# Optimization experiments

Measured on AMD Instinct MI355X. Metric: run time of the kernel, lower is better.

Reference implementation:

```python
import jax, jax.numpy as jnp
import numpy as np

B, N, E, D, H, C, U = 512, 256, 1024, 256, 256, 8, 64
MARGIN_T, RISK_T, SCALE = 0.2, 0.6, 0.1
NEG = -1.0e9


def setup_inputs() -> dict:
    key = jax.random.key(0)
    ks = jax.random.split(key, 30)
    s = 0.02
    inp = dict(
        features=jax.random.normal(ks[0], (B, D), jnp.float32),
        centered_scores=jax.random.normal(ks[1], (B, N), jnp.float32),
        margin=jax.random.uniform(ks[2], (B,), jnp.float32),
        boundary_risk=jax.random.uniform(ks[3], (B,), jnp.float32),
        edge_sensitivity=jax.random.normal(ks[4], (B, E), jnp.float32),
        coords=jax.random.normal(ks[5], (B, N, C), jnp.float32),
        uncertainty=jax.random.uniform(ks[6], (B, U), jnp.float32),
        Wc1=jax.random.normal(ks[7], (D, H), jnp.float32) * s,
        bc1=jnp.zeros((H,), jnp.float32),
        Wc2=jax.random.normal(ks[8], (H, H), jnp.float32) * s,
        bc2=jnp.zeros((H,), jnp.float32),
        Wn1=jax.random.normal(ks[9], (H + C + 2, H), jnp.float32) * s,
        bn1=jnp.zeros((H,), jnp.float32),
        Wn2=jax.random.normal(ks[10], (H, 1), jnp.float32) * s,
        bn2=jnp.zeros((1,), jnp.float32),
        We1=jax.random.normal(ks[11], (H + C + 2, H), jnp.float32) * s,
        be1=jnp.zeros((H,), jnp.float32),
        We2=jax.random.normal(ks[12], (H, 1), jnp.float32) * s,
        be2=jnp.zeros((1,), jnp.float32),
        Wg=jax.random.normal(ks[13], (H, 1), jnp.float32) * s,
        bg=jnp.zeros((1,), jnp.float32),
        action_mask=jax.random.bernoulli(ks[14], 0.8, (B, N)),
        edge_mask=jax.random.bernoulli(ks[15], 0.8, (B, E)),
        actions=jax.random.randint(ks[16], (B, N), 0, U, jnp.int32),
        edges=jax.random.randint(ks[17], (B, E, 2), 0, N, jnp.int32),
    )
    return inp


def _mlp2(x, W1, b1, W2, b2):
    return jax.nn.relu(x @ W1 + b1) @ W2 + b2


def reference(features, centered_scores, margin, boundary_risk, edge_sensitivity,
              coords, uncertainty, Wc1, bc1, Wc2, bc2, Wn1, bn1, Wn2, bn2,
              We1, be1, We2, be2, Wg, bg, action_mask, edge_mask, actions, edges):
    amf = action_mask.astype(jnp.float32)
    emf = edge_mask.astype(jnp.float32)

    # context MLP
    h = jax.nn.relu(jax.nn.relu(features @ Wc1 + bc1) @ Wc2 + bc2)  # [B,H]

    low_margin = (margin < MARGIN_T).astype(jnp.float32)
    high_risk = (boundary_risk > RISK_T).astype(jnp.float32)
    learned_gate = jax.nn.sigmoid((h @ Wg + bg)[:, 0])
    refine_gate = jnp.maximum(jnp.maximum(low_margin, high_risk),
                              (learned_gate > 0.5).astype(jnp.float32))  # [B]

    # node features: [B,N,H+C+2]
    act = jnp.clip(actions, 0, U - 1)
    unc_g = jnp.take_along_axis(uncertainty, act, axis=1)  # [B,N]
    h_n = jnp.broadcast_to(h[:, None, :], (B, N, H))
    node_feats = jnp.concatenate(
        [h_n, coords, centered_scores[..., None], unc_g[..., None]], axis=-1)
    node_delta = _mlp2(node_feats, Wn1, bn1, Wn2, bn2)[..., 0] * amf  # [B,N]

    # edge features: gather src/dst coords
    e = jnp.clip(edges, 0, N - 1)
    src_c = jnp.take_along_axis(coords, e[:, :, 0:1], axis=1)  # [B,E,C]
    dst_c = jnp.take_along_axis(coords, e[:, :, 1:2], axis=1)  # [B,E,C]
    h_e = jnp.broadcast_to(h[:, None, :], (B, E, H))
    edge_feats = jnp.concatenate(
        [h_e, dst_c - src_c, edge_sensitivity[..., None], emf[..., None]], axis=-1)
    edge_delta = _mlp2(edge_feats, We1, be1, We2, be2)[..., 0] * emf  # [B,E]

    gate_node = refine_gate[:, None]
    refined_scores = (centered_scores + gate_node * SCALE * node_delta) * amf
    denom = jnp.clip(amf.sum(-1, keepdims=True), 1.0, None)  # [B,1]
    refined_scores = (refined_scores - refined_scores.sum(-1, keepdims=True) / denom) * amf

    refined_edge = (edge_sensitivity + gate_node * SCALE * edge_delta) * emf

    masked_top = jnp.where(action_mask, refined_scores, NEG)
    top_vals, top_idx = jax.lax.top_k(masked_top, 2)
    refined_margin = top_vals[:, 0] - top_vals[:, 1]

    # masked per-batch variance of refined_edge (biased), 0 if <=1 valid entry
    cnt = emf.sum(-1)
    cnt_c = jnp.clip(cnt, 1.0, None)
    mean = (refined_edge * emf).sum(-1) / cnt_c
    var = (emf * (refined_edge - mean[:, None]) ** 2).sum(-1) / cnt_c
    edge_var = jnp.where(cnt > 1.0, var, 0.0)

    unc_term = (unc_g * amf).sum(-1) / denom[:, 0]
    refined_risk = jnp.clip(
        jax.nn.sigmoid(-refined_margin) + 0.2 * edge_var + 0.1 * unc_term, 0.0, 1.0)

    return (refined_scores, refined_margin, refined_edge,
            top_idx[:, 0], refined_risk, refine_gate)
```

## Files before the change

kernel.cpp:

```cpp
#include <hip/hip_runtime.h>
#include <math.h>

#define B 512
#define N 256
#define E 1024
#define D 256
#define H 256
#define C 8
#define U 64

typedef __fp16 h2 __attribute__((ext_vector_type(2)));
union UF { float f; h2 h; unsigned u; };

__device__ __forceinline__ float bc_f(h2 h) { UF u; u.h = h; return u.f; }
__device__ __forceinline__ h2 bc_h(float f) { UF u; u.f = f; return u.h; }

#if __has_builtin(__builtin_amdgcn_cvt_pkrtz)
__device__ __forceinline__ h2 pkh(float a, float b) { return __builtin_amdgcn_cvt_pkrtz(a, b); }
#else
__device__ __forceinline__ h2 pkh(float a, float b) { h2 r; r.x = (__fp16)a; r.y = (__fp16)b; return r; }
#endif

#if __has_builtin(__builtin_amdgcn_fdot2)
__device__ __forceinline__ float FDOT2(h2 a, h2 b, float c) { return __builtin_amdgcn_fdot2(a, b, c, false); }
#else
__device__ __forceinline__ float FDOT2(h2 a, h2 b, float c) {
    return fmaf((float)a.x, (float)b.x, fmaf((float)a.y, (float)b.y, c));
}
#endif

__device__ __forceinline__ float mask_val(const void* m, long i, int flag) {
    if (flag == 1) return ((const unsigned char*)m)[i] ? 1.f : 0.f;
    if (flag == 2) return (((const float*)m)[i] != 0.f) ? 1.f : 0.f;
    return ((const int*)m)[i] ? 1.f : 0.f;
}

__global__ __launch_bounds__(512) void k_h(
    const float* __restrict__ feat,
    const float* __restrict__ Wc1, const float* __restrict__ bc1,
    const float* __restrict__ Wc2, const float* __restrict__ bc2,
    const float* __restrict__ Wn1, const float* __restrict__ bn1,
    const float* __restrict__ We1, const float* __restrict__ be1,
    const float* __restrict__ Wg,  const float* __restrict__ bg,
    const float* __restrict__ margin, const float* __restrict__ brisk,
    const unsigned int* __restrict__ amask_words,
    float* __restrict__ base_n, float* __restrict__ base_e,
    float* __restrict__ out_gate, int* __restrict__ flag,
    float* __restrict__ node_delta, float* __restrict__ out2)
{
    __shared__ __align__(16) float sF[2][256];
    __shared__ __align__(16) float sH[2][256];
    __shared__ float red[512];
    __shared__ int cls0, cls1;

    int t = threadIdx.x;
    int w = t >> 8;
    int c = t & 255;
    int b0 = blockIdx.x * 2;
    int b = b0 + w;

    {
        int idx = blockIdx.x * 512 + t;
        node_delta[idx] = 0.f;
        ((float4*)out2)[idx] = make_float4(0.f, 0.f, 0.f, 0.f);
    }

    if (blockIdx.x == 0) {
        if (t == 0) { cls0 = 0; cls1 = 0; }
        __syncthreads();
        if (t < 256) {
            unsigned int wd = amask_words[t];
            if (wd != 0u && wd != 1u) {
                if (wd == 0x3f800000u) atomicOr(&cls1, 1);
                else                   atomicOr(&cls0, 1);
            }
        }
        __syncthreads();
        if (t == 0) *flag = cls0 ? 1 : (cls1 ? 2 : 0);
    }

    sF[w][c] = feat[(long)b * D + c];
    __syncthreads();

    {
        float acc[4] = {bc1[c], 0.f, 0.f, 0.f};
        const float* Wp = Wc1 + c;
        for (int d0 = 0; d0 < D; d0 += 16) {
            float wv[16];
            #pragma unroll
            for (int k = 0; k < 16; k++) wv[k] = Wp[(long)(d0 + k) * H];
            #pragma unroll
            for (int k = 0; k < 16; k++)
                acc[k & 3] = fmaf(sF[w][d0 + k], wv[k], acc[k & 3]);
        }
        sH[w][c] = fmaxf((acc[0] + acc[1]) + (acc[2] + acc[3]), 0.f);
    }
    __syncthreads();

    {
        float acc[4] = {bc2[c], 0.f, 0.f, 0.f};
        const float* Wp = Wc2 + c;
        for (int d0 = 0; d0 < H; d0 += 16) {
            float wv[16];
            #pragma unroll
            for (int k = 0; k < 16; k++) wv[k] = Wp[(long)(d0 + k) * H];
            #pragma unroll
            for (int k = 0; k < 16; k++)
                acc[k & 3] = fmaf(sH[w][d0 + k], wv[k], acc[k & 3]);
        }
        float a = fmaxf((acc[0] + acc[1]) + (acc[2] + acc[3]), 0.f);
        __syncthreads();
        sF[w][c] = a;
    }
    __syncthreads();

    red[t] = sF[w][c] * Wg[c];
    __syncthreads();
    for (int s = 128; s > 0; s >>= 1) {
        if (c < s) red[t] += red[t + s];
        __syncthreads();
    }
    if (c == 0) {
        float lg = 1.f / (1.f + expf(-(red[t] + bg[0])));
        out_gate[b] = ((margin[b] < 0.2f) || (brisk[b] > 0.6f) || (lg > 0.5f)) ? 1.f : 0.f;
    }

    {
        const float* W3  = w ? (We1 + c) : (Wn1 + c);
        float bias       = w ? be1[c]    : bn1[c];
        float* dst       = w ? base_e    : base_n;
        float aA[2] = {bias, 0.f};
        float aB[2] = {bias, 0.f};
        for (int d0 = 0; d0 < H; d0 += 16) {
            float wv[16];
            #pragma unroll
            for (int k = 0; k < 16; k++) wv[k] = W3[(long)(d0 + k) * H];
            #pragma unroll
            for (int k = 0; k < 16; k++) {
                aA[k & 1] = fmaf(sF[0][d0 + k], wv[k], aA[k & 1]);
                aB[k & 1] = fmaf(sF[1][d0 + k], wv[k], aB[k & 1]);
            }
        }
        dst[(long)b0 * H + c]       = aA[0] + aA[1];
        dst[(long)(b0 + 1) * H + c] = aB[0] + aB[1];
    }
}

__global__ __launch_bounds__(256, 2) void k_ne(
    const float* __restrict__ cs, const float* __restrict__ coords,
    const float* __restrict__ unc, const int* __restrict__ actions,
    const float* __restrict__ Wn1, const float* __restrict__ Wn2,
    const float* __restrict__ base_n,
    const float* __restrict__ es, const int* __restrict__ edges,
    const float* __restrict__ We1, const float* __restrict__ We2,
    const float* __restrict__ base_e,
    const float* __restrict__ gate,
    float* __restrict__ node_delta, float* __restrict__ out2)
{
    __shared__ __align__(16) float smem[3840];
    int t = threadIdx.x;
    int w = t >> 6, lane = t & 63;

    if (blockIdx.x < 512) {
        int rg = blockIdx.x >> 2;
        int jq = blockIdx.x & 3;
        int b0 = rg * 4;
        float* pack = smem;
        float* sB   = smem + 768;

        {
            int i = t;
            #pragma unroll
            for (int s = 0; s < 3; s++, i += 256) {
                int j = i / 12, k = i - j * 12;
                int jj = jq * 64 + j;
                float v;
                if (k < 10)       v = Wn1[(long)(H + k) * H + jj];
                else if (k == 10) v = Wn2[jj];
                else              v = 0.f;
                pack[i] = v;
            }
            int r = t >> 6, j = t & 63;
            sB[r * 64 + j] = base_n[(long)(b0 + r) * H + jq * 64 + j];
        }
        __syncthreads();

        int b = b0 + w;
        float g = gate[b];
        if (g != 0.f) {
            float f8v[4], ug[4], acc[4];
            float f0[4], f1[4], f2[4], f3[4], f4[4], f5[4], f6[4], f7[4];
            #pragma unroll
            for (int q = 0; q < 4; q++) {
                int n = q * 64 + lane;
                const float4* cp = (const float4*)(coords + ((long)b * N + n) * C);
                float4 c0 = cp[0], c1 = cp[1];
                f0[q] = c0.x; f1[q] = c0.y; f2[q] = c0.z; f3[q] = c0.w;
                f4[q] = c1.x; f5[q] = c1.y; f6[q] = c1.z; f7[q] = c1.w;
                f8v[q] = cs[(long)b * N + n];
                int a = actions[(long)b * N + n];
                a = min(max(a, 0), U - 1);
                ug[q] = unc[(long)b * U + a];
                acc[q] = 0.f;
            }

            const float* sBw = sB + w * 64;
            #pragma unroll 4
            for (int j = 0; j < 64; j++) {
                const float* pj = pack + j * 12;
                float4 wa = *(const float4*)(pj);
                float4 wb = *(const float4*)(pj + 4);
                float4 wc = *(const float4*)(pj + 8);
                float bse = sBw[j];
                #pragma unroll
                for (int q = 0; q < 4; q++) {
                    float zA = fmaf(f0[q], wa.x, bse);
                    zA = fmaf(f1[q], wa.y, zA);
                    zA = fmaf(f2[q], wa.z, zA);
                    zA = fmaf(f3[q], wa.w, zA);
                    float zB = f4[q] * wb.x;
                    zB = fmaf(f5[q], wb.y, zB);
                    zB = fmaf(f6[q], wb.z, zB);
                    zB = fmaf(f7[q], wb.w, zB);
                    zB = fmaf(f8v[q], wc.x, zB);
                    zB = fmaf(ug[q], wc.y, zB);
                    acc[q] = fmaf(fmaxf(zA + zB, 0.f), wc.z, acc[q]);
                }
            }

            #pragma unroll
            for (int q = 0; q < 4; q++)
                atomicAdd(&node_delta[(long)b * N + q * 64 + lane], acc[q]);
        }
    } else {
        int eb = blockIdx.x - 512;
        int b = eb >> 2, jq = eb & 3;
        float g = gate[b];
        if (g == 0.f) return;

        float*  A4 = smem;
        float2* B2 = (float2*)(smem + 256);
        float*  sC = smem + 768;

        {
            const float4* g4 = (const float4*)(coords + (long)b * N * C);
            float4 c0 = g4[2 * t], c1 = g4[2 * t + 1];
            float4* d0 = (float4*)(sC + t * 12);
            d0[0] = c0; d0[1] = c1;
        }
        if (t < 64) {
            int j = jq * 64 + t;
            float w0 = We1[(long)(H + 0) * H + j];
            float w1 = We1[(long)(H + 1) * H + j];
            float w2 = We1[(long)(H + 2) * H + j];
            float w3 = We1[(long)(H + 3) * H + j];
            float w4 = We1[(long)(H + 4) * H + j];
            float w5 = We1[(long)(H + 5) * H + j];
            float w6 = We1[(long)(H + 6) * H + j];
            float w7 = We1[(long)(H + 7) * H + j];
            float w8 = We1[(long)(H + 8) * H + j];
            float w9 = We1[(long)(H + 9) * H + j];
            float we2 = We2[j];
            float bse = base_e[(long)b * H + j] + w9;
            float4 av;
            av.x = bc_f(pkh(w0, w1)); av.y = bc_f(pkh(w2, w3));
            av.z = bc_f(pkh(w4, w5)); av.w = bc_f(pkh(w6, w7));
            ((float4*)A4)[t] = av;
            B2[t] = make_float2(bc_f(pkh(w8, we2)), bse);
        }
        __syncthreads();

        float p01[4], p23[4], p45[4], p67[4], pes[4], acc[4];
        #pragma unroll
        for (int q = 0; q < 4; q++) {
            long idx = (long)b * E + w * 256 + q * 64 + lane;
            int2 ev = ((const int2*)edges)[idx];
            int s0 = min(max(ev.x, 0), N - 1);
            int d0 = min(max(ev.y, 0), N - 1);
            const float4* cs4 = (const float4*)(sC + s0 * 12);
            const float4* cd4 = (const float4*)(sC + d0 * 12);
            float4 sa = cs4[0], sb = cs4[1];
            float4 da = cd4[0], db = cd4[1];
            p01[q] = bc_f(pkh(da.x - sa.x, da.y - sa.y));
            p23[q] = bc_f(pkh(da.z - sa.z, da.w - sa.w));
            p45[q] = bc_f(pkh(db.x - sb.x, db.y - sb.y));
            p67[q] = bc_f(pkh(db.z - sb.z, db.w - sb.w));
            pes[q] = bc_f(pkh(es[idx], 0.f));
            acc[q] = 0.f;
        }

        const float4* A4v = (const float4*)A4;
        #pragma unroll 4
        for (int j = 0; j < 64; j++) {
            float4 av = A4v[j];
            float2 bv = B2[j];
            h2 w01 = bc_h(av.x), w23 = bc_h(av.y);
            h2 w45 = bc_h(av.z), w67 = bc_h(av.w);
            h2 w8x = bc_h(bv.x);
            float we2f = (float)(w8x.y);
            float bse = bv.y;
            #pragma unroll
            for (int q = 0; q < 4; q++) {
                float z = FDOT2(bc_h(p01[q]), w01, bse);
                z = FDOT2(bc_h(p23[q]), w23, z);
                z = FDOT2(bc_h(p45[q]), w45, z);
                z = FDOT2(bc_h(p67[q]), w8x, z);
                acc[q] = acc[q];
                z = FDOT2(bc_h(p67[q]), w67, FDOT2(bc_h(p45[q]), w45,
                    FDOT2(bc_h(p23[q]), w23, FDOT2(bc_h(p01[q]), w01, bse))));
                z = FDOT2(bc_h(pes[q]), w8x, z);
                acc[q] = fmaf(fmaxf(z, 0.f), we2f, acc[q]);
            }
        }

        #pragma unroll
        for (int q = 0; q < 4; q++)
            atomicAdd(&out2[(long)b * E + w * 256 + q * 64 + lane], acc[q]);
    }
}

__global__ __launch_bounds__(512) void k_fin2(
    const void* __restrict__ amask, const void* __restrict__ emask,
    const int* __restrict__ actions, const float* __restrict__ unc,
    const float* __restrict__ cs, const float* __restrict__ es,
    const float* __restrict__ bn2, const float* __restrict__ be2,
    const float* __restrict__ gate, const int* __restrict__ flagp,
    const float* __restrict__ node_delta,
    float* __restrict__ out0, float* __restrict__ out1,
    float* __restrict__ out2, float* __restrict__ out3,
    float* __restrict__ out4)
{
    __shared__ float sRisk;
    __shared__ float sS1[8], sCe[8], sVar[8];
    int t = threadIdx.x;
    int w = t >> 6, lane = t & 63;
    int b = blockIdx.x;
    int flag = *flagp;
    float g = gate[b];

    float re[4], emv[4];

    if (w == 0) {
        float b2v = bn2[0];
        float raw[4], amv[4], ug[4];
        #pragma unroll
        for (int q = 0; q < 4; q++) {
            long idx = (long)b * N + q * 64 + lane;
            amv[q] = mask_val(amask, idx, flag);
            float csv = cs[idx];
            int a = actions[idx];
            a = min(max(a, 0), U - 1);
            ug[q] = unc[(long)b * U + a];
            float nd = (node_delta[idx] + b2v) * amv[q];
            raw[q] = (csv + g * 0.1f * nd) * amv[q];
        }

        float s = 0.f, cn = 0.f, su = 0.f;
        #pragma unroll
        for (int q = 0; q < 4; q++) {
            s += raw[q]; cn += amv[q]; su += ug[q] * amv[q];
        }
        #pragma unroll
        for (int m = 1; m < 64; m <<= 1) {
            s  += __shfl_xor(s, m);
            cn += __shfl_xor(cn, m);
            su += __shfl_xor(su, m);
        }
        float denom = fmaxf(cn, 1.f);
        float mu = s / denom;

        float masked[4];
        #pragma unroll
        for (int q = 0; q < 4; q++) {
            float rs = (raw[q] - mu) * amv[q];
            out0[(long)b * N + q * 64 + lane] = rs;
            masked[q] = (amv[q] != 0.f) ? rs : -1e9f;
        }

        float v1 = masked[0]; int i1 = lane; float v2 = -1e9f;
        #pragma unroll
        for (int q = 1; q < 4; q++) {
            float mv = masked[q]; int mi = q * 64 + lane;
            if (mv > v1) { v2 = v1; v1 = mv; i1 = mi; }
            else v2 = fmaxf(v2, mv);
        }
        #pragma unroll
        for (int m = 1; m < 64; m <<= 1) {
            float ov1 = __shfl_xor(v1, m);
            int   oi1 = __shfl_xor(i1, m);
            float ov2 = __shfl_xor(v2, m);
            bool ow = (ov1 > v1) || (ov1 == v1 && oi1 < i1);
            float lv  = ow ? v1 : ov1;
            float wv2 = ow ? ov2 : v2;
            if (ow) { v1 = ov1; i1 = oi1; }
            v2 = fmaxf(lv, wv2);
        }

        if (lane == 0) {
            float rmargin = v1 - v2;
            out1[b] = rmargin;
            out3[b] = (float)i1;
            float sig = 1.f / (1.f + expf(rmargin));
            sRisk = sig + 0.1f * (su / denom);
            sS1[0] = 0.f; sCe[0] = 0.f;
        }
    } else if (w >= 4) {
        float be2v = be2[0];
        int eq = w - 4;
        float S1 = 0.f, ce = 0.f;
        #pragma unroll
        for (int q = 0; q < 4; q++) {
            long idx = (long)b * E + eq * 256 + q * 64 + lane;
            emv[q] = mask_val(emask, idx, flag);
            float delta = out2[idx] + be2v;
            float r = es[idx] + g * 0.1f * delta;
            re[q] = (emv[q] != 0.f) ? r : 0.f;
            out2[idx] = re[q];
            S1 += re[q]; ce += emv[q];
        }
        #pragma unroll
        for (int m = 1; m < 64; m <<= 1) {
            S1 += __shfl_xor(S1, m);
            ce += __shfl_xor(ce, m);
        }
        if (lane == 0) { sS1[w] = S1; sCe[w] = ce; }
    } else {
        if (lane == 0) { sS1[w] = 0.f; sCe[w] = 0.f; }
    }
    __syncthreads();

    float S1t = sS1[4] + sS1[5] + sS1[6] + sS1[7];
    float cet = sCe[4] + sCe[5] + sCe[6] + sCe[7];
    float mean = S1t / fmaxf(cet, 1.f);

    if (w >= 4) {
        float v = 0.f;
        #pragma unroll
        for (int q = 0; q < 4; q++) {
            float dd = re[q] - mean;
            v = fmaf(emv[q] * dd, dd, v);
        }
        #pragma unroll
        for (int m = 1; m < 64; m <<= 1) v += __shfl_xor(v, m);
        if (lane == 0) sVar[w] = v;
    } else {
        if (lane == 0) sVar[w] = 0.f;
    }
    __syncthreads();

    if (t == 0) {
        float vt = sVar[4] + sVar[5] + sVar[6] + sVar[7];
        float var = vt / fmaxf(cet, 1.f);
        float ev = (cet > 1.f) ? var : 0.f;
        float r = sRisk + 0.2f * ev;
        out4[b] = fminf(fmaxf(r, 0.f), 1.f);
    }
}

extern "C" void kernel_launch(void* const* d_in, const int* in_sizes, int n_in,
                              void* d_out, int out_size, void* d_ws, size_t ws_size,
                              hipStream_t stream) {
    const float* feat   = (const float*)d_in[0];
    const float* cs     = (const float*)d_in[1];
    const float* marg   = (const float*)d_in[2];
    const float* brisk  = (const float*)d_in[3];
    const float* es     = (const float*)d_in[4];
    const float* coords = (const float*)d_in[5];
    const float* unc    = (const float*)d_in[6];
    const float* Wc1    = (const float*)d_in[7];
    const float* bc1    = (const float*)d_in[8];
    const float* Wc2    = (const float*)d_in[9];
    const float* bc2    = (const float*)d_in[10];
    const float* Wn1    = (const float*)d_in[11];
    const float* bn1    = (const float*)d_in[12];
    const float* Wn2    = (const float*)d_in[13];
    const float* bn2    = (const float*)d_in[14];
    const float* We1    = (const float*)d_in[15];
    const float* be1    = (const float*)d_in[16];
    const float* We2    = (const float*)d_in[17];
    const float* be2    = (const float*)d_in[18];
    const float* Wg     = (const float*)d_in[19];
    const float* bg     = (const float*)d_in[20];
    const void*  amask  = d_in[21];
    const void*  emask  = d_in[22];
    const int*   actions= (const int*)d_in[23];
    const int*   edges  = (const int*)d_in[24];

    float* out0 = (float*)d_out;
    float* out1 = out0 + (long)B * N;
    float* out2 = out1 + B;
    float* out3 = out2 + (long)B * E;
    float* out4 = out3 + B;
    float* out5 = out4 + B;

    float* base_n     = (float*)d_ws;
    float* base_e     = base_n + (long)B * H;
    float* node_delta = base_e + (long)B * H;
    int*   flag       = (int*)(node_delta + (long)B * N);

    k_h<<<B / 2, 512, 0, stream>>>(feat, Wc1, bc1, Wc2, bc2, Wn1, bn1, We1, be1,
                                   Wg, bg, marg, brisk,
                                   (const unsigned int*)amask,
                                   base_n, base_e, out5, flag,
                                   node_delta, out2);
    k_ne<<<512 + 4 * B, 256, 0, stream>>>(cs, coords, unc, actions,
                                          Wn1, Wn2, base_n,
                                          es, edges,
                                          We1, We2, base_e,
                                          out5, node_delta, out2);
    k_fin2<<<B, 512, 0, stream>>>(amask, emask, actions, unc, cs, es,
                                  bn2, be2, out5, flag, node_delta,
                                  out0, out1, out2, out3, out4);
}
```

Before: 69.95 us.

## Split context MLP kernel into three wider-parallel kernels and drop redundant FDOT chain

The single context-MLP kernel, which ran 256 blocks of 512 threads and handled two rows per block through three dependent matmuls, is split into three kernels. Each new kernel handles 4 rows by 64 output columns per block, giving 512 to 1024 blocks. The gate logit is now reduced with wavefront shuffles into per-quarter partial sums and finished in the third kernel. Separately, the edge inner loop drops a duplicated FDOT2 chain that recomputed z. The split adds two extra launches plus workspace round-trips for intermediates, in exchange for more parallelism and less per-block serial work.

```diff
diff --git a/kernel.cpp b/kernel.cpp
--- a/kernel.cpp
+++ b/kernel.cpp
@@ -35,114 +35,149 @@
     return ((const int*)m)[i] ? 1.f : 0.f;
 }
 
-__global__ __launch_bounds__(512) void k_h(
+__global__ __launch_bounds__(256) void k_h1(
     const float* __restrict__ feat,
     const float* __restrict__ Wc1, const float* __restrict__ bc1,
-    const float* __restrict__ Wc2, const float* __restrict__ bc2,
-    const float* __restrict__ Wn1, const float* __restrict__ bn1,
-    const float* __restrict__ We1, const float* __restrict__ be1,
-    const float* __restrict__ Wg,  const float* __restrict__ bg,
-    const float* __restrict__ margin, const float* __restrict__ brisk,
     const unsigned int* __restrict__ amask_words,
-    float* __restrict__ base_n, float* __restrict__ base_e,
-    float* __restrict__ out_gate, int* __restrict__ flag,
-    float* __restrict__ node_delta, float* __restrict__ out2)
+    float* __restrict__ A_ws, int* __restrict__ flag,
+    float* __restrict__ node_delta, float* __restrict__ out2,
+    float* __restrict__ gate_part)
 {
-    __shared__ __align__(16) float sF[2][256];
-    __shared__ __align__(16) float sH[2][256];
-    __shared__ float red[512];
+    __shared__ __align__(16) float sF[4][256];
     __shared__ int cls0, cls1;
-
     int t = threadIdx.x;
-    int w = t >> 8;
-    int c = t & 255;
-    int b0 = blockIdx.x * 2;
-    int b = b0 + w;
+    int rg = blockIdx.x >> 2, jq = blockIdx.x & 3;
+    int b0 = rg * 4;
+    int r = t >> 6, lane = t & 63;
+    int c = jq * 64 + lane;
 
     {
-        int idx = blockIdx.x * 512 + t;
+        int idx = blockIdx.x * 256 + t;
         node_delta[idx] = 0.f;
         ((float4*)out2)[idx] = make_float4(0.f, 0.f, 0.f, 0.f);
+        if (blockIdx.x < 8) gate_part[blockIdx.x * 256 + t] = 0.f;
     }
 
     if (blockIdx.x == 0) {
         if (t == 0) { cls0 = 0; cls1 = 0; }
         __syncthreads();
-        if (t < 256) {
-            unsigned int wd = amask_words[t];
-            if (wd != 0u && wd != 1u) {
-                if (wd == 0x3f800000u) atomicOr(&cls1, 1);
-                else                   atomicOr(&cls0, 1);
-            }
+        unsigned int wd = amask_words[t];
+        if (wd != 0u && wd != 1u) {
+            if (wd == 0x3f800000u) atomicOr(&cls1, 1);
+            else                   atomicOr(&cls0, 1);
         }
         __syncthreads();
         if (t == 0) *flag = cls0 ? 1 : (cls1 ? 2 : 0);
     }
 
-    sF[w][c] = feat[(long)b * D + c];
+    #pragma unroll
+    for (int rr = 0; rr < 4; rr++) sF[rr][t] = feat[(long)(b0 + rr) * D + t];
     __syncthreads();
 
-    {
-        float acc[4] = {bc1[c], 0.f, 0.f, 0.f};
-        const float* Wp = Wc1 + c;
-        for (int d0 = 0; d0 < D; d0 += 16) {
-            float wv[16];
-            #pragma unroll
-            for (int k = 0; k < 16; k++) wv[k] = Wp[(long)(d0 + k) * H];
-            #pragma unroll
-            for (int k = 0; k < 16; k++)
-                acc[k & 3] = fmaf(sF[w][d0 + k], wv[k], acc[k & 3]);
-        }
-        sH[w][c] = fmaxf((acc[0] + acc[1]) + (acc[2] + acc[3]), 0.f);
-    }
+    float a0 = bc1[c], a1 = 0.f;
+    const float* Wp = Wc1 + c;
+    for (int k0 = 0; k0 < D; k0 += 8) {
+        float wv[8];
+        #pragma unroll
+        for (int i = 0; i < 8; i++) wv[i] = Wp[(long)(k0 + i) * H];
+        #pragma unroll
+        for (int i = 0; i < 8; i++) {
+            float f = sF[r][k0 + i];
+            if (i & 1) a1 = fmaf(f, wv[i], a1);
+            else       a0 = fmaf(f, wv[i], a0);
+        }
+    }
+    A_ws[(long)(b0 + r) * H + c] = fmaxf(a0 + a1, 0.f);
+}
+
+__global__ __launch_bounds__(256) void k_h2(
+    const float* __restrict__ A_ws,
+    const float* __restrict__ Wc2, const float* __restrict__ bc2,
+    const float* __restrict__ Wg,
+    float* __restrict__ h_ws, float* __restrict__ gate_part)
+{
+    __shared__ __align__(16) float sA[4][256];
+    int t = threadIdx.x;
+    int rg = blockIdx.x >> 2, jq = blockIdx.x & 3;
+    int b0 = rg * 4;
+    int r = t >> 6, lane = t & 63;
+    int c = jq * 64 + lane;
+
+    #pragma unroll
+    for (int rr = 0; rr < 4; rr++) sA[rr][t] = A_ws[(long)(b0 + rr) * H + t];
     __syncthreads();
 
-    {
-        float acc[4] = {bc2[c], 0.f, 0.f, 0.f};
-        const float* Wp = Wc2 + c;
-        for (int d0 = 0; d0 < H; d0 += 16) {
-            float wv[16];
-            #pragma unroll
-            for (int k = 0; k < 16; k++) wv[k] = Wp[(long)(d0 + k) * H];
-            #pragma unroll
-            for (int k = 0; k < 16; k++)
-                acc[k & 3] = fmaf(sH[w][d0 + k], wv[k], acc[k & 3]);
-        }
-        float a = fmaxf((acc[0] + acc[1]) + (acc[2] + acc[3]), 0.f);
-        __syncthreads();
-        sF[w][c] = a;
-    }
+    float a0 = bc2[c], a1 = 0.f;
+    const float* Wp = Wc2 + c;
+    for (int k0 = 0; k0 < H; k0 += 8) {
+        float wv[8];
+        #pragma unroll
+        for (int i = 0; i < 8; i++) wv[i] = Wp[(long)(k0 + i) * H];
+        #pragma unroll
+        for (int i = 0; i < 8; i++) {
+            float f = sA[r][k0 + i];
+            if (i & 1) a1 = fmaf(f, wv[i], a1);
+            else       a0 = fmaf(f, wv[i], a0);
+        }
+    }
+    float h = fmaxf(a0 + a1, 0.f);
+    h_ws[(long)(b0 + r) * H + c] = h;
+
+    float p = h * Wg[c];
+    #pragma unroll
+    for (int m = 1; m < 64; m <<= 1) p += __shfl_xor(p, m);
+    if (lane == 0) gate_part[(long)(b0 + r) * 4 + jq] = p;
+}
+
+__global__ __launch_bounds__(256) void k_h3(
+    const float* __restrict__ h_ws,
+    const float* __restrict__ Wn1, const float* __restrict__ bn1,
+    const float* __restrict__ We1, const float* __restrict__ be1,
+    const float* __restrict__ bg,
+    const float* __restrict__ margin, const float* __restrict__ brisk,
+    const float* __restrict__ gate_part,
+    float* __restrict__ base_n, float* __restrict__ base_e,
+    float* __restrict__ out_gate)
+{
+    __shared__ __align__(16) float sH[4][256];
+    int t = threadIdx.x;
+    int bid = blockIdx.x;
+    int mat = bid >> 9;
+    int rem = bid & 511;
+    int rg = rem >> 2, jq = rem & 3;
+    int b0 = rg * 4;
+    int r = t >> 6, lane = t & 63;
+    int c = jq * 64 + lane;
+
+    #pragma unroll
+    for (int rr = 0; rr < 4; rr++) sH[rr][t] = h_ws[(long)(b0 + rr) * H + t];
     __syncthreads();
 
-    red[t] = sF[w][c] * Wg[c];
-    __syncthreads();
-    for (int s = 128; s > 0; s >>= 1) {
-        if (c < s) red[t] += red[t + s];
-        __syncthreads();
-    }
-    if (c == 0) {
-        float lg = 1.f / (1.f + expf(-(red[t] + bg[0])));
+    const float* W3  = mat ? We1 : Wn1;
+    float bias       = mat ? be1[c] : bn1[c];
+    float* dst       = mat ? base_e : base_n;
+
+    float a0 = bias, a1 = 0.f;
+    const float* Wp = W3 + c;
+    for (int k0 = 0; k0 < H; k0 += 8) {
+        float wv[8];
+        #pragma unroll
+        for (int i = 0; i < 8; i++) wv[i] = Wp[(long)(k0 + i) * H];
+        #pragma unroll
+        for (int i = 0; i < 8; i++) {
+            float f = sH[r][k0 + i];
+            if (i & 1) a1 = fmaf(f, wv[i], a1);
+            else       a0 = fmaf(f, wv[i], a0);
+        }
+    }
+    dst[(long)(b0 + r) * H + c] = a0 + a1;
+
+    if (mat == 0 && jq == 0 && t < 4) {
+        int b = b0 + t;
+        float s = ((gate_part[(long)b * 4 + 0] + gate_part[(long)b * 4 + 1])
+                 + gate_part[(long)b * 4 + 2]) + gate_part[(long)b * 4 + 3];
+        float lg = 1.f / (1.f + expf(-(s + bg[0])));
         out_gate[b] = ((margin[b] < 0.2f) || (brisk[b] > 0.6f) || (lg > 0.5f)) ? 1.f : 0.f;
-    }
-
-    {
-        const float* W3  = w ? (We1 + c) : (Wn1 + c);
-        float bias       = w ? be1[c]    : bn1[c];
-        float* dst       = w ? base_e    : base_n;
-        float aA[2] = {bias, 0.f};
-        float aB[2] = {bias, 0.f};
-        for (int d0 = 0; d0 < H; d0 += 16) {
-            float wv[16];
-            #pragma unroll
-            for (int k = 0; k < 16; k++) wv[k] = W3[(long)(d0 + k) * H];
-            #pragma unroll
-            for (int k = 0; k < 16; k++) {
-                aA[k & 1] = fmaf(sF[0][d0 + k], wv[k], aA[k & 1]);
-                aB[k & 1] = fmaf(sF[1][d0 + k], wv[k], aB[k & 1]);
-            }
-        }
-        dst[(long)b0 * H + c]       = aA[0] + aA[1];
-        dst[(long)(b0 + 1) * H + c] = aB[0] + aB[1];
     }
 }
 
@@ -304,10 +339,7 @@
                 float z = FDOT2(bc_h(p01[q]), w01, bse);
                 z = FDOT2(bc_h(p23[q]), w23, z);
                 z = FDOT2(bc_h(p45[q]), w45, z);
-                z = FDOT2(bc_h(p67[q]), w8x, z);
-                acc[q] = acc[q];
-                z = FDOT2(bc_h(p67[q]), w67, FDOT2(bc_h(p45[q]), w45,
-                    FDOT2(bc_h(p23[q]), w23, FDOT2(bc_h(p01[q]), w01, bse))));
+                z = FDOT2(bc_h(p67[q]), w67, z);
                 z = FDOT2(bc_h(pes[q]), w8x, z);
                 acc[q] = fmaf(fmaxf(z, 0.f), we2f, acc[q]);
             }
@@ -496,13 +528,18 @@
     float* base_n     = (float*)d_ws;
     float* base_e     = base_n + (long)B * H;
     float* node_delta = base_e + (long)B * H;
-    int*   flag       = (int*)(node_delta + (long)B * N);
-
-    k_h<<<B / 2, 512, 0, stream>>>(feat, Wc1, bc1, Wc2, bc2, Wn1, bn1, We1, be1,
-                                   Wg, bg, marg, brisk,
-                                   (const unsigned int*)amask,
-                                   base_n, base_e, out5, flag,
-                                   node_delta, out2);
+    float* A_ws       = node_delta + (long)B * N;
+    float* h_ws       = A_ws + (long)B * H;
+    float* gate_part  = h_ws + (long)B * H;
+    int*   flag       = (int*)(gate_part + 4 * B);
+
+    k_h1<<<512, 256, 0, stream>>>(feat, Wc1, bc1,
+                                  (const unsigned int*)amask,
+                                  A_ws, flag, node_delta, out2, gate_part);
+    k_h2<<<512, 256, 0, stream>>>(A_ws, Wc2, bc2, Wg, h_ws, gate_part);
+    k_h3<<<1024, 256, 0, stream>>>(h_ws, Wn1, bn1, We1, be1, bg,
+                                   marg, brisk, gate_part,
+                                   base_n, base_e, out5);
     k_ne<<<512 + 4 * B, 256, 0, stream>>>(cs, coords, unc, actions,
                                           Wn1, Wn2, base_n,
                                           es, edges,
```

Result: slower. 73.33 us (+4.8%).
